# Performance work log

Hardware: AMD Instinct MI355X
Metric: run time of the kernel (lower is better)

## Reference

```python
import jax, jax.numpy as jnp
import numpy as np
from math import sqrt

MEM_SIZE = 1024
MEM_DIM = 256


def setup_inputs() -> dict:
    key = jax.random.key(0)
    k1, k2, k3 = jax.random.split(key, 3)
    x = jax.random.normal(k1, (8, 256, 64, 64), dtype=jnp.float32)
    mask = jax.random.randint(k2, (8, 1, 64, 64), 0, 2).astype(jnp.bool_)
    mem = jax.random.normal(k3, (1, MEM_DIM, MEM_SIZE), dtype=jnp.float32)
    return {"x": x, "mask": mask, "mem": mem}


def reference(x, mask, mem):
    # masked-detach blend: x.detach() * ~mask + x * mask
    x = jnp.where(mask, x, jax.lax.stop_gradient(x))
    B, K, H, W = x.shape
    xf = x.reshape(B, K, H * W)            # (B, K, N)
    m = mem[0]                              # (K, M) with M = mem_size
    # logits = m_key @ x / sqrt(K)  -> (B, M, N)
    logits = jnp.einsum('km,bkn->bmn', m, xf) / sqrt(K)
    attn = jax.nn.softmax(logits, axis=1)   # softmax over memory axis
    # out = m @ attn -> (B, K, N)
    out = jnp.einsum('km,bmn->bkn', m, attn).reshape(B, K, H, W)
    return (out, logits)
```

## Files before the change

### kernel.cpp

```cpp
#include <hip/hip_runtime.h>
#include <stdint.h>


typedef __attribute__((ext_vector_type(8))) __bf16 bf16x8;
typedef __attribute__((ext_vector_type(4))) float f32x4;

#define BQ 8
#define KD 256
#define MD 1024
#define ND 4096
#define NT 32

__device__ __forceinline__ unsigned short bf16_rne(float f) {
    union { float f; uint32_t u; } c; c.f = f;
    uint32_t u = c.u;
    uint32_t r = (u + 0x7FFFu + ((u >> 16) & 1u)) >> 16;
    return (unsigned short)r;
}

__global__ void prep_mem(const float* __restrict__ mem,
                         unsigned short* __restrict__ mT,
                         unsigned short* __restrict__ mR) {
    const int k = blockIdx.x;
    const int t = threadIdx.x;
    float4 v = reinterpret_cast<const float4*>(mem + (size_t)k * MD)[t];
    unsigned short h0 = bf16_rne(v.x), h1 = bf16_rne(v.y),
                   h2 = bf16_rne(v.z), h3 = bf16_rne(v.w);
    reinterpret_cast<uint2*>(mR + (size_t)k * MD)[t] =
        make_uint2((uint32_t)h0 | ((uint32_t)h1 << 16),
                   (uint32_t)h2 | ((uint32_t)h3 << 16));
    const int mm = t * 4;
    mT[(size_t)(mm + 0) * KD + k] = h0;
    mT[(size_t)(mm + 1) * KD + k] = h1;
    mT[(size_t)(mm + 2) * KD + k] = h2;
    mT[(size_t)(mm + 3) * KD + k] = h3;
}

__global__ __launch_bounds__(512, 4) void fused_attn_mem(
    const float* __restrict__ x,
    const unsigned short* __restrict__ mT,
    const unsigned short* __restrict__ mR,
    float* __restrict__ out,
    float* __restrict__ logits)
{
    __shared__ __align__(16) char lds[65536];
    float* red_max = (float*)(lds + 32768);
    float* red_sum = (float*)(lds + 33792);

    const int tid = threadIdx.x;
    const int w   = tid >> 6;
    const int l   = tid & 63;
    const int l15 = l & 15;
    const int l4  = l >> 4;

    const int bid = blockIdx.x;
    const int b   = bid >> 7;
    const int n0  = (bid & 127) * NT;

    {
        const float* xb = x + (size_t)b * KD * ND + n0;
        const int k  = tid >> 1;
        const int nh = (tid & 1) * 16;
        const float4* src = reinterpret_cast<const float4*>(xb + (size_t)k * ND + nh);
        float4 v0 = src[0], v1 = src[1], v2 = src[2], v3 = src[3];
        float vals[16] = {v0.x, v0.y, v0.z, v0.w, v1.x, v1.y, v1.z, v1.w,
                          v2.x, v2.y, v2.z, v2.w, v3.x, v3.y, v3.z, v3.w};
        #pragma unroll
        for (int j = 0; j < 16; ++j) {
            const int n = nh + j;
            const int off = n * 512 + (((k >> 3) ^ (n & 7)) << 4) + (k & 7) * 2;
            *(unsigned short*)(lds + off) = bf16_rne(vals[j]);
        }
    }
    __syncthreads();

    f32x4 acc[8][2];
    #pragma unroll
    for (int rt = 0; rt < 8; ++rt)
        #pragma unroll
        for (int ct = 0; ct < 2; ++ct)
            acc[rt][ct] = (f32x4){0.f, 0.f, 0.f, 0.f};

    #pragma unroll
    for (int ks = 0; ks < 8; ++ks) {
        const int kk = ks * 32 + l4 * 8;
        bf16x8 bfr[2];
        #pragma unroll
        for (int ct = 0; ct < 2; ++ct) {
            const int n = ct * 16 + l15;
            const int off = n * 512 + (((kk >> 3) ^ (n & 7)) << 4);
            bfr[ct] = *(const bf16x8*)(lds + off);
        }
        #pragma unroll
        for (int rt = 0; rt < 8; ++rt) {
            const int row = w * 128 + rt * 16 + l15;
            const bf16x8 afr = *(const bf16x8*)(mT + (size_t)row * KD + kk);
            acc[rt][0] = __builtin_amdgcn_mfma_f32_16x16x32_bf16(afr, bfr[0], acc[rt][0], 0, 0, 0);
            acc[rt][1] = __builtin_amdgcn_mfma_f32_16x16x32_bf16(afr, bfr[1], acc[rt][1], 0, 0, 0);
        }
    }

    float lmax[2] = {-3e38f, -3e38f};
    #pragma unroll
    for (int rt = 0; rt < 8; ++rt) {
        #pragma unroll
        for (int ct = 0; ct < 2; ++ct) {
            f32x4 v = acc[rt][ct] * 0.0625f;
            acc[rt][ct] = v;
            lmax[ct] = fmaxf(lmax[ct], fmaxf(fmaxf(v[0], v[1]), fmaxf(v[2], v[3])));
        }
    }

    {
        char* sw = lds + 34816 + w * 2048;
        float* lg = logits + (size_t)b * MD * ND + n0;
        #pragma unroll
        for (int rt = 0; rt < 8; ++rt) {
            #pragma unroll
            for (int ct = 0; ct < 2; ++ct) {
                const int n = ct * 16 + l15;
                #pragma unroll
                for (int r = 0; r < 4; ++r) {
                    const int mloc = l4 * 4 + r;
                    const int off = mloc * 128 + (((n >> 2) ^ (mloc & 7)) << 4) + ((n & 3) << 2);
                    *(float*)(sw + off) = acc[rt][ct][r];
                }
            }
            __asm__ volatile("s_waitcnt lgkmcnt(0)" ::: "memory");
            __builtin_amdgcn_sched_barrier(0);
            #pragma unroll
            for (int half = 0; half < 2; ++half) {
                const int mloc = (l >> 3) + half * 8;
                const int q = l & 7;
                const f32x4 v = *(const f32x4*)(sw + mloc * 128 + ((q ^ (mloc & 7)) << 4));
                *(f32x4*)(lg + (size_t)(w * 128 + rt * 16 + mloc) * ND + q * 4) = v;
            }
            __asm__ volatile("s_waitcnt lgkmcnt(0)" ::: "memory");
            __builtin_amdgcn_sched_barrier(0);
        }
    }

    #pragma unroll
    for (int ct = 0; ct < 2; ++ct) {
        float m = lmax[ct];
        m = fmaxf(m, __shfl_xor(m, 16, 64));
        m = fmaxf(m, __shfl_xor(m, 32, 64));
        lmax[ct] = m;
    }
    if (l < 16) {
        red_max[(w * 2 + 0) * 16 + l] = lmax[0];
        red_max[(w * 2 + 1) * 16 + l] = lmax[1];
    }
    __syncthreads();

    float cmax[2];
    #pragma unroll
    for (int ct = 0; ct < 2; ++ct) {
        float m = -3e38f;
        #pragma unroll
        for (int ww = 0; ww < 8; ++ww)
            m = fmaxf(m, red_max[(ww * 2 + ct) * 16 + l15]);
        cmax[ct] = m;
    }

    float lsum[2] = {0.f, 0.f};
    #pragma unroll
    for (int rt = 0; rt < 8; ++rt) {
        #pragma unroll
        for (int ct = 0; ct < 2; ++ct) {
            f32x4 v = acc[rt][ct];
            v[0] = __expf(v[0] - cmax[ct]);
            v[1] = __expf(v[1] - cmax[ct]);
            v[2] = __expf(v[2] - cmax[ct]);
            v[3] = __expf(v[3] - cmax[ct]);
            lsum[ct] += (v[0] + v[1]) + (v[2] + v[3]);
            acc[rt][ct] = v;
        }
    }
    #pragma unroll
    for (int ct = 0; ct < 2; ++ct) {
        float s = lsum[ct];
        s += __shfl_xor(s, 16, 64);
        s += __shfl_xor(s, 32, 64);
        lsum[ct] = s;
    }
    if (l < 16) {
        red_sum[(w * 2 + 0) * 16 + l] = lsum[0];
        red_sum[(w * 2 + 1) * 16 + l] = lsum[1];
    }
    __syncthreads();

    float rs[2];
    #pragma unroll
    for (int ct = 0; ct < 2; ++ct) {
        float s = 0.f;
        #pragma unroll
        for (int ww = 0; ww < 8; ++ww)
            s += red_sum[(ww * 2 + ct) * 16 + l15];
        rs[ct] = 1.0f / s;
    }
    __syncthreads();

    #pragma unroll
    for (int rt = 0; rt < 8; ++rt) {
        #pragma unroll
        for (int ct = 0; ct < 2; ++ct) {
            f32x4 v = acc[rt][ct];
            unsigned short h0 = bf16_rne(v[0] * rs[ct]);
            unsigned short h1 = bf16_rne(v[1] * rs[ct]);
            unsigned short h2 = bf16_rne(v[2] * rs[ct]);
            unsigned short h3 = bf16_rne(v[3] * rs[ct]);
            const int m0 = w * 128 + rt * 16 + l4 * 4;
            const int n  = ct * 16 + l15;
            const int off = n * 2048 + (((m0 >> 3) ^ (n & 7)) << 4) + (m0 & 7) * 2;
            *(uint2*)(lds + off) = make_uint2((uint32_t)h0 | ((uint32_t)h1 << 16),
                                              (uint32_t)h2 | ((uint32_t)h3 << 16));
        }
    }
    __syncthreads();

    f32x4 acc2[2][2];
    #pragma unroll
    for (int rtile = 0; rtile < 2; ++rtile)
        #pragma unroll
        for (int ct = 0; ct < 2; ++ct)
            acc2[rtile][ct] = (f32x4){0.f, 0.f, 0.f, 0.f};

    #pragma unroll 4
    for (int ks = 0; ks < 32; ++ks) {
        const int mk = ks * 32 + l4 * 8;
        bf16x8 b2[2];
        #pragma unroll
        for (int ct = 0; ct < 2; ++ct) {
            const int n = ct * 16 + l15;
            const int off = n * 2048 + (((mk >> 3) ^ (n & 7)) << 4);
            b2[ct] = *(const bf16x8*)(lds + off);
        }
        #pragma unroll
        for (int rtile = 0; rtile < 2; ++rtile) {
            const bf16x8 a2 = *(const bf16x8*)(mR + (size_t)(w * 32 + rtile * 16 + l15) * MD + mk);
            acc2[rtile][0] = __builtin_amdgcn_mfma_f32_16x16x32_bf16(a2, b2[0], acc2[rtile][0], 0, 0, 0);
            acc2[rtile][1] = __builtin_amdgcn_mfma_f32_16x16x32_bf16(a2, b2[1], acc2[rtile][1], 0, 0, 0);
        }
    }

    float* ob = out + (size_t)b * KD * ND + n0;
    #pragma unroll
    for (int rtile = 0; rtile < 2; ++rtile) {
        #pragma unroll
        for (int ct = 0; ct < 2; ++ct) {
            const int n  = ct * 16 + l15;
            const int r0 = w * 32 + rtile * 16 + l4 * 4;
            ob[(size_t)(r0 + 0) * ND + n] = acc2[rtile][ct][0];
            ob[(size_t)(r0 + 1) * ND + n] = acc2[rtile][ct][1];
            ob[(size_t)(r0 + 2) * ND + n] = acc2[rtile][ct][2];
            ob[(size_t)(r0 + 3) * ND + n] = acc2[rtile][ct][3];
        }
    }
}

extern "C" void kernel_launch(void* const* d_in, const int* in_sizes, int n_in,
                              void* d_out, int out_size, void* d_ws, size_t ws_size,
                              hipStream_t stream) {
    (void)in_sizes; (void)n_in; (void)out_size; (void)ws_size;
    const float* x   = (const float*)d_in[0];
    const float* mem = (const float*)d_in[2];

    float* out    = (float*)d_out;
    float* logits = (float*)d_out + (size_t)BQ * KD * ND;

    unsigned short* mT = (unsigned short*)d_ws;
    unsigned short* mR = mT + (size_t)MD * KD;

    prep_mem<<<dim3(256), dim3(256), 0, stream>>>(mem, mT, mR);
    fused_attn_mem<<<dim3(BQ * (ND / NT)), dim3(512), 0, stream>>>(x, mT, mR, out, logits);
}
```

Before: 138.7 us.

## Double column tile to 64 with 1024-thread blocks and coalesced output staging

Each block now covers 64 spatial columns with 16 waves and 160KB of dynamic LDS, so every mem row fetched from global is reused across twice as many columns. The block index is remapped to group strips, and the output GEMM is restaged through LDS so stores are 16-byte coalesced rows instead of scattered scalar writes. The logits staging layout changes to padded rows. In exchange, occupancy drops to one block per CU because of the large LDS footprint, and there are more barriers among 16 waves.

```diff
diff --git a/kernel.cpp b/kernel.cpp
--- a/kernel.cpp
+++ b/kernel.cpp
@@ -9,7 +9,7 @@
 #define KD 256
 #define MD 1024
 #define ND 4096
-#define NT 32
+#define NT 64
 
 __device__ __forceinline__ unsigned short bf16_rne(float f) {
     union { float f; uint32_t u; } c; c.f = f;
@@ -36,16 +36,16 @@
     mT[(size_t)(mm + 3) * KD + k] = h3;
 }
 
-__global__ __launch_bounds__(512, 4) void fused_attn_mem(
+__global__ __launch_bounds__(1024, 4) void fused_attn_mem(
     const float* __restrict__ x,
     const unsigned short* __restrict__ mT,
     const unsigned short* __restrict__ mR,
     float* __restrict__ out,
     float* __restrict__ logits)
 {
-    __shared__ __align__(16) char lds[65536];
-    float* red_max = (float*)(lds + 32768);
-    float* red_sum = (float*)(lds + 33792);
+    extern __shared__ char lds[];
+    float* red_max = (float*)(lds);
+    float* red_sum = (float*)(lds + 4096);
 
     const int tid = threadIdx.x;
     const int w   = tid >> 6;
@@ -54,57 +54,61 @@
     const int l4  = l >> 4;
 
     const int bid = blockIdx.x;
-    const int b   = bid >> 7;
-    const int n0  = (bid & 127) * NT;
+    const int g   = bid & 7;
+    const int j   = bid >> 3;
+    const int strip = g * 8 + (j & 7);
+    const int b     = j >> 3;
+    const int n0    = strip * NT;
 
     {
         const float* xb = x + (size_t)b * KD * ND + n0;
-        const int k  = tid >> 1;
-        const int nh = (tid & 1) * 16;
+        const int k  = tid >> 2;
+        const int nh = (tid & 3) * 16;
         const float4* src = reinterpret_cast<const float4*>(xb + (size_t)k * ND + nh);
         float4 v0 = src[0], v1 = src[1], v2 = src[2], v3 = src[3];
         float vals[16] = {v0.x, v0.y, v0.z, v0.w, v1.x, v1.y, v1.z, v1.w,
                           v2.x, v2.y, v2.z, v2.w, v3.x, v3.y, v3.z, v3.w};
         #pragma unroll
-        for (int j = 0; j < 16; ++j) {
-            const int n = nh + j;
+        for (int jj = 0; jj < 16; ++jj) {
+            const int n = nh + jj;
             const int off = n * 512 + (((k >> 3) ^ (n & 7)) << 4) + (k & 7) * 2;
-            *(unsigned short*)(lds + off) = bf16_rne(vals[j]);
-        }
-    }
-    __syncthreads();
-
-    f32x4 acc[8][2];
-    #pragma unroll
-    for (int rt = 0; rt < 8; ++rt)
-        #pragma unroll
-        for (int ct = 0; ct < 2; ++ct)
+            *(unsigned short*)(lds + off) = bf16_rne(vals[jj]);
+        }
+    }
+    __syncthreads();
+
+    f32x4 acc[4][4];
+    #pragma unroll
+    for (int rt = 0; rt < 4; ++rt)
+        #pragma unroll
+        for (int ct = 0; ct < 4; ++ct)
             acc[rt][ct] = (f32x4){0.f, 0.f, 0.f, 0.f};
 
     #pragma unroll
     for (int ks = 0; ks < 8; ++ks) {
         const int kk = ks * 32 + l4 * 8;
-        bf16x8 bfr[2];
-        #pragma unroll
-        for (int ct = 0; ct < 2; ++ct) {
+        bf16x8 bfr[4];
+        #pragma unroll
+        for (int ct = 0; ct < 4; ++ct) {
             const int n = ct * 16 + l15;
             const int off = n * 512 + (((kk >> 3) ^ (n & 7)) << 4);
             bfr[ct] = *(const bf16x8*)(lds + off);
         }
         #pragma unroll
-        for (int rt = 0; rt < 8; ++rt) {
-            const int row = w * 128 + rt * 16 + l15;
+        for (int rt = 0; rt < 4; ++rt) {
+            const int row = w * 64 + rt * 16 + l15;
             const bf16x8 afr = *(const bf16x8*)(mT + (size_t)row * KD + kk);
-            acc[rt][0] = __builtin_amdgcn_mfma_f32_16x16x32_bf16(afr, bfr[0], acc[rt][0], 0, 0, 0);
-            acc[rt][1] = __builtin_amdgcn_mfma_f32_16x16x32_bf16(afr, bfr[1], acc[rt][1], 0, 0, 0);
-        }
-    }
-
-    float lmax[2] = {-3e38f, -3e38f};
-    #pragma unroll
-    for (int rt = 0; rt < 8; ++rt) {
-        #pragma unroll
-        for (int ct = 0; ct < 2; ++ct) {
+            #pragma unroll
+            for (int ct = 0; ct < 4; ++ct)
+                acc[rt][ct] = __builtin_amdgcn_mfma_f32_16x16x32_bf16(afr, bfr[ct], acc[rt][ct], 0, 0, 0);
+        }
+    }
+
+    float lmax[4] = {-3e38f, -3e38f, -3e38f, -3e38f};
+    #pragma unroll
+    for (int rt = 0; rt < 4; ++rt) {
+        #pragma unroll
+        for (int ct = 0; ct < 4; ++ct) {
             f32x4 v = acc[rt][ct] * 0.0625f;
             acc[rt][ct] = v;
             lmax[ct] = fmaxf(lmax[ct], fmaxf(fmaxf(v[0], v[1]), fmaxf(v[2], v[3])));
@@ -112,28 +116,26 @@
     }
 
     {
-        char* sw = lds + 34816 + w * 2048;
+        char* sw = lds + 32768 + w * 4608;
         float* lg = logits + (size_t)b * MD * ND + n0;
         #pragma unroll
-        for (int rt = 0; rt < 8; ++rt) {
-            #pragma unroll
-            for (int ct = 0; ct < 2; ++ct) {
+        for (int rt = 0; rt < 4; ++rt) {
+            #pragma unroll
+            for (int ct = 0; ct < 4; ++ct) {
                 const int n = ct * 16 + l15;
                 #pragma unroll
                 for (int r = 0; r < 4; ++r) {
                     const int mloc = l4 * 4 + r;
-                    const int off = mloc * 128 + (((n >> 2) ^ (mloc & 7)) << 4) + ((n & 3) << 2);
-                    *(float*)(sw + off) = acc[rt][ct][r];
+                    *(float*)(sw + mloc * 272 + n * 4) = acc[rt][ct][r];
                 }
             }
             __asm__ volatile("s_waitcnt lgkmcnt(0)" ::: "memory");
             __builtin_amdgcn_sched_barrier(0);
             #pragma unroll
-            for (int half = 0; half < 2; ++half) {
-                const int mloc = (l >> 3) + half * 8;
-                const int q = l & 7;
-                const f32x4 v = *(const f32x4*)(sw + mloc * 128 + ((q ^ (mloc & 7)) << 4));
-                *(f32x4*)(lg + (size_t)(w * 128 + rt * 16 + mloc) * ND + q * 4) = v;
+            for (int p = 0; p < 4; ++p) {
+                const int mloc = p * 4 + l4;
+                const f32x4 v = *(const f32x4*)(sw + mloc * 272 + l15 * 16);
+                *(f32x4*)(lg + (size_t)(w * 64 + rt * 16 + mloc) * ND + l15 * 4) = v;
             }
             __asm__ volatile("s_waitcnt lgkmcnt(0)" ::: "memory");
             __builtin_amdgcn_sched_barrier(0);
@@ -141,33 +143,35 @@
     }
 
     #pragma unroll
-    for (int ct = 0; ct < 2; ++ct) {
+    for (int ct = 0; ct < 4; ++ct) {
         float m = lmax[ct];
         m = fmaxf(m, __shfl_xor(m, 16, 64));
         m = fmaxf(m, __shfl_xor(m, 32, 64));
         lmax[ct] = m;
     }
+    __syncthreads();
     if (l < 16) {
-        red_max[(w * 2 + 0) * 16 + l] = lmax[0];
-        red_max[(w * 2 + 1) * 16 + l] = lmax[1];
-    }
-    __syncthreads();
-
-    float cmax[2];
-    #pragma unroll
-    for (int ct = 0; ct < 2; ++ct) {
+        #pragma unroll
+        for (int ct = 0; ct < 4; ++ct)
+            red_max[(w * 4 + ct) * 16 + l] = lmax[ct];
+    }
+    __syncthreads();
+
+    float cmax[4];
+    #pragma unroll
+    for (int ct = 0; ct < 4; ++ct) {
         float m = -3e38f;
         #pragma unroll
-        for (int ww = 0; ww < 8; ++ww)
-            m = fmaxf(m, red_max[(ww * 2 + ct) * 16 + l15]);
+        for (int ww = 0; ww < 16; ++ww)
+            m = fmaxf(m, red_max[(ww * 4 + ct) * 16 + l15]);
         cmax[ct] = m;
     }
 
-    float lsum[2] = {0.f, 0.f};
-    #pragma unroll
-    for (int rt = 0; rt < 8; ++rt) {
-        #pragma unroll
-        for (int ct = 0; ct < 2; ++ct) {
+    float lsum[4] = {0.f, 0.f, 0.f, 0.f};
+    #pragma unroll
+    for (int rt = 0; rt < 4; ++rt) {
+        #pragma unroll
+        for (int ct = 0; ct < 4; ++ct) {
             f32x4 v = acc[rt][ct];
             v[0] = __expf(v[0] - cmax[ct]);
             v[1] = __expf(v[1] - cmax[ct]);
@@ -178,83 +182,86 @@
         }
     }
     #pragma unroll
-    for (int ct = 0; ct < 2; ++ct) {
+    for (int ct = 0; ct < 4; ++ct) {
         float s = lsum[ct];
         s += __shfl_xor(s, 16, 64);
         s += __shfl_xor(s, 32, 64);
         lsum[ct] = s;
     }
     if (l < 16) {
-        red_sum[(w * 2 + 0) * 16 + l] = lsum[0];
-        red_sum[(w * 2 + 1) * 16 + l] = lsum[1];
-    }
-    __syncthreads();
-
-    float rs[2];
-    #pragma unroll
-    for (int ct = 0; ct < 2; ++ct) {
+        #pragma unroll
+        for (int ct = 0; ct < 4; ++ct)
+            red_sum[(w * 4 + ct) * 16 + l] = lsum[ct];
+    }
+    __syncthreads();
+
+    float rs[4];
+    #pragma unroll
+    for (int ct = 0; ct < 4; ++ct) {
         float s = 0.f;
         #pragma unroll
-        for (int ww = 0; ww < 8; ++ww)
-            s += red_sum[(ww * 2 + ct) * 16 + l15];
+        for (int ww = 0; ww < 16; ++ww)
+            s += red_sum[(ww * 4 + ct) * 16 + l15];
         rs[ct] = 1.0f / s;
     }
-    __syncthreads();
-
-    #pragma unroll
-    for (int rt = 0; rt < 8; ++rt) {
-        #pragma unroll
-        for (int ct = 0; ct < 2; ++ct) {
+
+    #pragma unroll
+    for (int rt = 0; rt < 4; ++rt) {
+        #pragma unroll
+        for (int ct = 0; ct < 4; ++ct) {
             f32x4 v = acc[rt][ct];
             unsigned short h0 = bf16_rne(v[0] * rs[ct]);
             unsigned short h1 = bf16_rne(v[1] * rs[ct]);
             unsigned short h2 = bf16_rne(v[2] * rs[ct]);
             unsigned short h3 = bf16_rne(v[3] * rs[ct]);
-            const int m0 = w * 128 + rt * 16 + l4 * 4;
+            const int m0 = w * 64 + rt * 16 + l4 * 4;
             const int n  = ct * 16 + l15;
-            const int off = n * 2048 + (((m0 >> 3) ^ (n & 7)) << 4) + (m0 & 7) * 2;
+            const int off = 32768 + n * 2048 + (((m0 >> 3) ^ (n & 7)) << 4) + (m0 & 7) * 2;
             *(uint2*)(lds + off) = make_uint2((uint32_t)h0 | ((uint32_t)h1 << 16),
                                               (uint32_t)h2 | ((uint32_t)h3 << 16));
         }
     }
     __syncthreads();
 
-    f32x4 acc2[2][2];
-    #pragma unroll
-    for (int rtile = 0; rtile < 2; ++rtile)
-        #pragma unroll
-        for (int ct = 0; ct < 2; ++ct)
-            acc2[rtile][ct] = (f32x4){0.f, 0.f, 0.f, 0.f};
-
+    f32x4 acc2[4];
+    #pragma unroll
+    for (int ct = 0; ct < 4; ++ct)
+        acc2[ct] = (f32x4){0.f, 0.f, 0.f, 0.f};
+
+    const unsigned short* arow = mR + (size_t)(w * 16 + l15) * MD;
     #pragma unroll 4
     for (int ks = 0; ks < 32; ++ks) {
         const int mk = ks * 32 + l4 * 8;
-        bf16x8 b2[2];
-        #pragma unroll
-        for (int ct = 0; ct < 2; ++ct) {
+        const bf16x8 a2 = *(const bf16x8*)(arow + mk);
+        #pragma unroll
+        for (int ct = 0; ct < 4; ++ct) {
             const int n = ct * 16 + l15;
-            const int off = n * 2048 + (((mk >> 3) ^ (n & 7)) << 4);
-            b2[ct] = *(const bf16x8*)(lds + off);
-        }
-        #pragma unroll
-        for (int rtile = 0; rtile < 2; ++rtile) {
-            const bf16x8 a2 = *(const bf16x8*)(mR + (size_t)(w * 32 + rtile * 16 + l15) * MD + mk);
-            acc2[rtile][0] = __builtin_amdgcn_mfma_f32_16x16x32_bf16(a2, b2[0], acc2[rtile][0], 0, 0, 0);
-            acc2[rtile][1] = __builtin_amdgcn_mfma_f32_16x16x32_bf16(a2, b2[1], acc2[rtile][1], 0, 0, 0);
-        }
-    }
-
-    float* ob = out + (size_t)b * KD * ND + n0;
-    #pragma unroll
-    for (int rtile = 0; rtile < 2; ++rtile) {
-        #pragma unroll
-        for (int ct = 0; ct < 2; ++ct) {
-            const int n  = ct * 16 + l15;
-            const int r0 = w * 32 + rtile * 16 + l4 * 4;
-            ob[(size_t)(r0 + 0) * ND + n] = acc2[rtile][ct][0];
-            ob[(size_t)(r0 + 1) * ND + n] = acc2[rtile][ct][1];
-            ob[(size_t)(r0 + 2) * ND + n] = acc2[rtile][ct][2];
-            ob[(size_t)(r0 + 3) * ND + n] = acc2[rtile][ct][3];
+            const int off = 32768 + n * 2048 + (((mk >> 3) ^ (n & 7)) << 4);
+            const bf16x8 b2 = *(const bf16x8*)(lds + off);
+            acc2[ct] = __builtin_amdgcn_mfma_f32_16x16x32_bf16(a2, b2, acc2[ct], 0, 0, 0);
+        }
+    }
+    __syncthreads();
+
+    {
+        char* sw = lds + 32768 + w * 4608;
+        float* ob = out + (size_t)b * KD * ND + n0;
+        #pragma unroll
+        for (int ct = 0; ct < 4; ++ct) {
+            const int n = ct * 16 + l15;
+            #pragma unroll
+            for (int r = 0; r < 4; ++r) {
+                const int rr = l4 * 4 + r;
+                *(float*)(sw + rr * 272 + n * 4) = acc2[ct][r];
+            }
+        }
+        __asm__ volatile("s_waitcnt lgkmcnt(0)" ::: "memory");
+        __builtin_amdgcn_sched_barrier(0);
+        #pragma unroll
+        for (int p = 0; p < 4; ++p) {
+            const int rr = p * 4 + l4;
+            const f32x4 v = *(const f32x4*)(sw + rr * 272 + l15 * 16);
+            *(f32x4*)(ob + (size_t)(w * 16 + rr) * ND + l15 * 4) = v;
         }
     }
 }
@@ -272,6 +279,13 @@
     unsigned short* mT = (unsigned short*)d_ws;
     unsigned short* mR = mT + (size_t)MD * KD;
 
+    static int lds_attr_set = 0;
+    if (!lds_attr_set) {
+        hipFuncSetAttribute(reinterpret_cast<const void*>(&fused_attn_mem),
+                            hipFuncAttributeMaxDynamicSharedMemorySize, 163840);
+        lds_attr_set = 1;
+    }
+
     prep_mem<<<dim3(256), dim3(256), 0, stream>>>(mem, mT, mR);
-    fused_attn_mem<<<dim3(BQ * (ND / NT)), dim3(512), 0, stream>>>(x, mT, mR, out, logits);
-}
+    fused_attn_mem<<<dim3(BQ * (ND / NT)), dim3(1024), 163840, stream>>>(x, mT, mR, out, logits);
+}
```

Measured after the change: 112.1 us. 1.24x faster.
